# Kernel optimization log

Hardware: AMD Instinct MI355X
Metric: run time of the kernel (lower is better)

The kernel has to match this reference:

```python
import jax, jax.numpy as jnp
import numpy as np

GROUPS = 32
EPS = 1e-5


def setup_inputs() -> dict:
    key = jax.random.key(0)
    ks = jax.random.split(key, 4)
    n, c, h, w = 4, 512, 64, 64
    x = jax.random.normal(ks[0], (n, c, h, w), dtype=jnp.float32)
    gn_scale = jnp.ones((c,), dtype=jnp.float32)
    gn_bias = jnp.zeros((c,), dtype=jnp.float32)
    w_in = jax.random.normal(ks[1], (3 * c, c), dtype=jnp.float32) * (1.0 / np.sqrt(c))
    b_in = jnp.zeros((3 * c,), dtype=jnp.float32)
    w_out = jax.random.normal(ks[2], (c, c), dtype=jnp.float32) * (1.0 / np.sqrt(c))
    b_out = jnp.zeros((c,), dtype=jnp.float32)
    return {"x": x, "gn_scale": gn_scale, "gn_bias": gn_bias,
            "w_in": w_in, "b_in": b_in, "w_out": w_out, "b_out": b_out}


def reference(x, gn_scale, gn_bias, w_in, b_in, w_out, b_out):
    n, c, h, w = x.shape
    # GroupNorm(32, c): normalize over (c//32, h, w) per group
    xg = x.reshape(n, GROUPS, -1)
    mean = xg.mean(axis=-1, keepdims=True)
    var = xg.var(axis=-1, keepdims=True)
    xn = ((xg - mean) * jax.lax.rsqrt(var + EPS)).reshape(n, c, h, w)
    xn = xn * gn_scale[:, None, None] + gn_bias[:, None, None]
    # [n, c, h, w] -> [n, hw, c]
    seq = xn.reshape(n, c, h * w).transpose(0, 2, 1)
    # fused qkv projection
    qkv = jnp.einsum('nsc,dc->nsd', seq, w_in) + b_in  # [n, hw, 3c]
    q, k, v = jnp.split(qkv, 3, axis=-1)
    # single head, head_dim = c
    scale = 1.0 / jnp.sqrt(jnp.asarray(c, dtype=x.dtype))
    scores = jnp.einsum('nsc,ntc->nst', q, k) * scale  # [n, hw, hw]
    attn = jax.nn.softmax(scores, axis=-1)
    out = jnp.einsum('nst,ntc->nsc', attn, v)
    out = jnp.einsum('nsc,dc->nsd', out, w_out) + b_out
    out = out.transpose(0, 2, 1).reshape(n, c, h, w)
    return out + x
```

## Files before the change

### kernel.cpp

```cpp
#include <hip/hip_runtime.h>
#include <hip/hip_bf16.h>

#define NBATCH 4
#define C 512
#define HW 4096
#define GROUPS 32
#define EPSV 1e-5f
#define ATTN_SCALE_L2 0.0637587085f

typedef short bf16x8 __attribute__((ext_vector_type(8)));
typedef float f32x4 __attribute__((ext_vector_type(4)));

__device__ __forceinline__ float bf(unsigned short u) {
  return __uint_as_float(((unsigned)u) << 16);
}
__device__ __forceinline__ unsigned short fb(float v) {
  __hip_bfloat16 h = __float2bfloat16(v);
  return *(unsigned short*)&h;
}
__device__ __forceinline__ bf16x8 frag_ld(const short* p) {
  return *(const bf16x8*)p;
}
#define MFMA(a, b, c) __builtin_amdgcn_mfma_f32_16x16x32_bf16((a), (b), (c), 0, 0, 0)

#define SCHED_FENCE() __builtin_amdgcn_sched_barrier(0)
#define BAR()                                   \
  do {                                          \
    asm volatile("" ::: "memory");              \
    SCHED_FENCE();                              \
    __builtin_amdgcn_s_barrier();               \
    SCHED_FENCE();                              \
    asm volatile("" ::: "memory");              \
  } while (0)
#define WAITV(N)                                                  \
  do {                                                            \
    asm volatile("s_waitcnt vmcnt(" #N ")" ::: "memory");         \
    SCHED_FENCE();                                                \
  } while (0)
#define WAITLGKM()                                                \
  do {                                                            \
    asm volatile("s_waitcnt lgkmcnt(0)" ::: "memory");            \
    SCHED_FENCE();                                                \
  } while (0)

__device__ __forceinline__ void gl_lds16(const short* g, short* l) {
  __builtin_amdgcn_global_load_lds(
      (const __attribute__((address_space(1))) unsigned int*)g,
      (__attribute__((address_space(3))) unsigned int*)l, 16, 0, 0);
}

__device__ __forceinline__ void unpack8(uint4 w, float* f) {
  f[0] = __uint_as_float(w.x << 16);
  f[1] = __uint_as_float(w.x & 0xFFFF0000u);
  f[2] = __uint_as_float(w.y << 16);
  f[3] = __uint_as_float(w.y & 0xFFFF0000u);
  f[4] = __uint_as_float(w.z << 16);
  f[5] = __uint_as_float(w.z & 0xFFFF0000u);
  f[6] = __uint_as_float(w.w << 16);
  f[7] = __uint_as_float(w.w & 0xFFFF0000u);
}

__device__ __forceinline__ bool detect_f32(const void* w_in) {
  const unsigned short* u = (const unsigned short*)w_in;
  bool f32 = false;
#pragma unroll
  for (int i = 0; i < 64; ++i) {
    float v = bf(u[i]);
    if (!(fabsf(v) < 1e3f)) f32 = true;
  }
  return f32;
}
__device__ __forceinline__ float ld(const void* p, size_t i, bool f32) {
  if (f32) return ((const float*)p)[i];
  return bf(((const unsigned short*)p)[i]);
}

__device__ __forceinline__ void stage_xn(short* xn, const void* x,
                                         const void* gsc, const void* gbi,
                                         const float* stats, int nn, int t0,
                                         bool f32) {
  const int tid = threadIdx.x;
  const int part = tid & 3, crel = tid >> 2;
  for (int c0 = 0; c0 < 512; c0 += 64) {
    int c = c0 + crel;
    float rr = stats[128 + nn * GROUPS + (c >> 4)];
    float mu = stats[nn * GROUPS + (c >> 4)];
    float scl = ld(gsc, c, f32) * rr;
    float sft = ld(gbi, c, f32) - mu * scl;
    float f[8];
    if (f32) {
      const float4* p = (const float4*)((const float*)x +
                                        ((size_t)(nn * C + c) << 12) + t0 + part * 8);
      float4 r0 = p[0], r1 = p[1];
      f[0] = r0.x; f[1] = r0.y; f[2] = r0.z; f[3] = r0.w;
      f[4] = r1.x; f[5] = r1.y; f[6] = r1.z; f[7] = r1.w;
    } else {
      uint4 raw = *(const uint4*)((const unsigned short*)x +
                                  ((size_t)(nn * C + c) << 12) + t0 + part * 8);
      unpack8(raw, f);
    }
#pragma unroll
    for (int j = 0; j < 8; ++j)
      xn[(part * 8 + j) * 520 + c] = (short)fb(f[j] * scl + sft);
  }
}

__global__ __launch_bounds__(256) void gn_stats_kernel(
    const void* __restrict__ x, const void* __restrict__ w_in,
    float* __restrict__ stats) {
  const bool f32 = detect_f32(w_in);
  const int b = blockIdx.x;
  const size_t base = (size_t)b << 16;
  float s = 0.f, ss = 0.f;
  for (int i = threadIdx.x; i < 65536; i += 256) {
    float v = ld(x, base + i, f32);
    s += v;
    ss += v * v;
  }
  __shared__ float rs[256], rq[256];
  rs[threadIdx.x] = s;
  rq[threadIdx.x] = ss;
  __syncthreads();
  for (int off = 128; off > 0; off >>= 1) {
    if (threadIdx.x < off) {
      rs[threadIdx.x] += rs[threadIdx.x + off];
      rq[threadIdx.x] += rq[threadIdx.x + off];
    }
    __syncthreads();
  }
  if (threadIdx.x == 0) {
    float m = rs[0] * (1.0f / 65536.0f);
    float var = rq[0] * (1.0f / 65536.0f) - m * m;
    stats[b] = m;
    stats[128 + b] = rsqrtf(var + EPSV);
  }
}

__global__ __launch_bounds__(256) void wconv_kernel(
    const void* __restrict__ w_in, const void* __restrict__ w_out,
    short* __restrict__ wbf) {
  const bool f32 = detect_f32(w_in);
  size_t i = ((size_t)blockIdx.x * 256 + threadIdx.x) * 4;
  const void* src;
  size_t off;
  if (i < 786432) {
    src = w_in;
    off = i;
  } else {
    src = w_out;
    off = i - 786432;
  }
  if (f32) {
    float4 v = *(const float4*)((const float*)src + off);
    uint2 u;
    u.x = (unsigned)fb(v.x) | ((unsigned)fb(v.y) << 16);
    u.y = (unsigned)fb(v.z) | ((unsigned)fb(v.w) << 16);
    *(uint2*)(wbf + i) = u;
  } else {
    *(uint2*)(wbf + i) = *(const uint2*)((const unsigned short*)src + off);
  }
}

__global__ __launch_bounds__(256) void kv_gemm_kernel(
    const void* __restrict__ x, const void* __restrict__ gsc,
    const void* __restrict__ gbi, const float* __restrict__ stats,
    const void* __restrict__ w_in, const void* __restrict__ b_in,
    const short* __restrict__ wbf, unsigned short* __restrict__ kvbase,
    int nn0) {
  const bool f32 = detect_f32(w_in);
  const int nn = nn0 + blockIdx.z;
  unsigned short* kbuf = kvbase + (size_t)blockIdx.z * 4194304;
  unsigned short* vbuf = kbuf + 2097152;
  __shared__ __align__(16) short xn[32 * 520];
  const int tid = threadIdx.x;
  const int wave = tid >> 6, lane = tid & 63, l15 = lane & 15, quad = lane >> 4;
  const int t0 = blockIdx.y * 32;
  const int proj = blockIdx.x >> 1;
  const int ehalf = blockIdx.x & 1;

  stage_xn(xn, x, gsc, gbi, stats, nn, t0, f32);
  __syncthreads();

  const int wrow = 512 + proj * 512 + ehalf * 256 + wave * 64;
  const int cbase = ehalf * 256 + wave * 64;

  f32x4 acc[4][2];
#pragma unroll
  for (int i = 0; i < 4; ++i) {
    acc[i][0] = {0.f, 0.f, 0.f, 0.f};
    acc[i][1] = {0.f, 0.f, 0.f, 0.f};
  }

  for (int kc = 0; kc < 16; ++kc) {
    bf16x8 b0f = frag_ld(xn + l15 * 520 + kc * 32 + quad * 8);
    bf16x8 b1f = frag_ld(xn + (16 + l15) * 520 + kc * 32 + quad * 8);
#pragma unroll
    for (int es = 0; es < 4; ++es) {
      bf16x8 a = frag_ld(wbf + (size_t)(wrow + es * 16 + l15) * 512 + kc * 32 + quad * 8);
      acc[es][0] = MFMA(a, b0f, acc[es][0]);
      acc[es][1] = MFMA(a, b1f, acc[es][1]);
    }
  }

#pragma unroll
  for (int es = 0; es < 4; ++es) {
    int bidx = wrow + es * 16 + quad * 4;
    float b0 = ld(b_in, bidx, f32), b1 = ld(b_in, bidx + 1, f32);
    float b2 = ld(b_in, bidx + 2, f32), b3 = ld(b_in, bidx + 3, f32);
    int ecol = cbase + es * 16 + quad * 4;
#pragma unroll
    for (int ts = 0; ts < 2; ++ts) {
      int t = t0 + ts * 16 + l15;
      float vr[4] = {acc[es][ts][0] + b0, acc[es][ts][1] + b1,
                     acc[es][ts][2] + b2, acc[es][ts][3] + b3};
      if (proj == 0) {
        int sw = (((ecol >> 3) ^ (t & 7)) << 3) | (ecol & 7);
        uint2 u;
        u.x = (unsigned)fb(vr[0]) | ((unsigned)fb(vr[1]) << 16);
        u.y = (unsigned)fb(vr[2]) | ((unsigned)fb(vr[3]) << 16);
        *(uint2*)(kbuf + (size_t)t * 512 + sw) = u;
      } else {
        size_t tb = (size_t)(t >> 5) * 16384;
        int trel = t & 31;
#pragma unroll
        for (int i = 0; i < 4; ++i) {
          int e = ecol + i;
          vbuf[tb + (size_t)e * 32 + ((((trel >> 3) ^ ((e >> 1) & 3)) << 3)) +
               (trel & 7)] = fb(vr[i]);
        }
      }
    }
  }
}

__global__ __launch_bounds__(256, 2) void flash32_kernel(
    const void* __restrict__ x, const void* __restrict__ gsc,
    const void* __restrict__ gbi, const float* __restrict__ stats,
    const void* __restrict__ w_in, const void* __restrict__ b_in,
    const short* __restrict__ wbf, const short* __restrict__ wbfo,
    const unsigned short* __restrict__ kvbase,
    const void* __restrict__ b_out, void* __restrict__ out, int nn0,
    int conc) {
  const bool f32 = detect_f32(w_in);
  int nn, t0, slot;
  if (conc) {
    int xcd = blockIdx.x & 7;
    nn = xcd >> 1;
    slot = nn;
    t0 = ((((xcd & 1) << 6) | (blockIdx.x >> 3))) << 5;
  } else {
    nn = nn0; slot = 0; t0 = blockIdx.x << 5;
  }
  const unsigned short* kbuf = kvbase + (size_t)slot * 4194304;
  const unsigned short* vbuf = kbuf + 2097152;

  __shared__ __align__(16) short lds[35200];
  short* RA = lds;
  short* RB = lds + 16640;
  short* Ps = lds + 33280;
  float* hmf = (float*)(lds + 34560);
  float* lbf = (float*)(lds + 35072);
  const int tid = threadIdx.x;
  const int wave = tid >> 6, lane = tid & 63, l15 = lane & 15, quad = lane >> 4;
  const int th = wave & 1;
  const int qh = wave >> 1;

  bf16x8 q[16];
  stage_xn(RA, x, gsc, gbi, stats, nn, t0, f32);
  __syncthreads();
  {
    f32x4 qacc[8][2];
#pragma unroll
    for (int i = 0; i < 8; ++i) {
      qacc[i][0] = {0.f, 0.f, 0.f, 0.f};
      qacc[i][1] = {0.f, 0.f, 0.f, 0.f};
    }
    for (int kc = 0; kc < 16; ++kc) {
      bf16x8 bx0 = frag_ld(RA + l15 * 520 + kc * 32 + quad * 8);
      bf16x8 bx1 = frag_ld(RA + (16 + l15) * 520 + kc * 32 + quad * 8);
#pragma unroll
      for (int es = 0; es < 8; ++es) {
        bf16x8 a = frag_ld(wbf + (size_t)(wave * 128 + es * 16 + l15) * 512 + kc * 32 + quad * 8);
        qacc[es][0] = MFMA(a, bx0, qacc[es][0]);
        qacc[es][1] = MFMA(a, bx1, qacc[es][1]);
      }
    }
#pragma unroll
    for (int es = 0; es < 8; ++es) {
      int e0 = wave * 128 + es * 16 + quad * 4;
      float b0 = ld(b_in, e0, f32), b1 = ld(b_in, e0 + 1, f32);
      float b2 = ld(b_in, e0 + 2, f32), b3 = ld(b_in, e0 + 3, f32);
#pragma unroll
      for (int ts = 0; ts < 2; ++ts) {
        int t = ts * 16 + l15;
        uint2 u;
        u.x = (unsigned)fb((qacc[es][ts][0] + b0) * ATTN_SCALE_L2) |
              ((unsigned)fb((qacc[es][ts][1] + b1) * ATTN_SCALE_L2) << 16);
        u.y = (unsigned)fb((qacc[es][ts][2] + b2) * ATTN_SCALE_L2) |
              ((unsigned)fb((qacc[es][ts][3] + b3) * ATTN_SCALE_L2) << 16);
        *(uint2*)(RB + t * 520 + e0) = u;
      }
    }
    __syncthreads();
#pragma unroll
    for (int kc = 0; kc < 16; ++kc)
      q[kc] = frag_ld(RB + (qh * 16 + l15) * 520 + kc * 32 + quad * 8);
    __syncthreads();
  }

#define STAGE_K(tk)                                                           \
  {                                                                           \
    const short* s_ = (const short*)kbuf + (size_t)(tk)*16384 + wave * 4096 + \
                      lane * 8;                                               \
    short* d_ = RA + wave * 4096;                                             \
    _Pragma("unroll") for (int i_ = 0; i_ < 8; ++i_)                          \
        gl_lds16(s_ + i_ * 512, d_ + i_ * 512);                               \
  }
#define STAGE_V(tk)                                                           \
  {                                                                           \
    const short* s_ = (const short*)vbuf + (size_t)(tk)*16384 + wave * 4096 + \
                      lane * 8;                                               \
    short* d_ = RB + wave * 4096;                                             \
    _Pragma("unroll") for (int i_ = 0; i_ < 8; ++i_)                          \
        gl_lds16(s_ + i_ * 512, d_ + i_ * 512);                               \
  }

  f32x4 o[2][8];
#pragma unroll
  for (int hh = 0; hh < 2; ++hh)
#pragma unroll
    for (int et = 0; et < 8; ++et) o[hh][et] = {0.f, 0.f, 0.f, 0.f};
  float mrow2[2] = {-3.0e38f, -3.0e38f};
  float lpart = 0.f;

  STAGE_K(0);
  STAGE_V(0);

  for (int tk = 0; tk < 128; ++tk) {
    WAITV(8);
    BAR();

    f32x4 sA = {0.f, 0.f, 0.f, 0.f}, sB = {0.f, 0.f, 0.f, 0.f};
    __builtin_amdgcn_s_setprio(1);
#pragma unroll
    for (int kc = 0; kc < 16; kc += 2) {
      int g0 = ((kc * 4 + quad) ^ (l15 & 7)) * 8;
      int g1 = (((kc + 1) * 4 + quad) ^ (l15 & 7)) * 8;
      bf16x8 kb0 = frag_ld(RA + (th * 16 + l15) * 512 + g0);
      bf16x8 kb1 = frag_ld(RA + (th * 16 + l15) * 512 + g1);
      sA = MFMA(kb0, q[kc], sA);
      sB = MFMA(kb1, q[kc + 1], sB);
    }
    __builtin_amdgcn_s_setprio(0);
    f32x4 s = sA + sB;
    float hm = fmaxf(fmaxf(s[0], s[1]), fmaxf(s[2], s[3]));
    hmf[th * 128 + (qh * 16 + l15) * 4 + quad] = hm;
    WAITLGKM();
    BAR();
    if (tk < 127) STAGE_K(tk + 1);

    float4 a0 = *(const float4*)&hmf[l15 * 4];
    float4 a1 = *(const float4*)&hmf[128 + l15 * 4];
    float4 c0 = *(const float4*)&hmf[(16 + l15) * 4];
    float4 c1 = *(const float4*)&hmf[128 + (16 + l15) * 4];
    float m0 = fmaxf(fmaxf(fmaxf(a0.x, a0.y), fmaxf(a0.z, a0.w)),
                     fmaxf(fmaxf(a1.x, a1.y), fmaxf(a1.z, a1.w)));
    float m1 = fmaxf(fmaxf(fmaxf(c0.x, c0.y), fmaxf(c0.z, c0.w)),
                     fmaxf(fmaxf(c1.x, c1.y), fmaxf(c1.z, c1.w)));
    bool grow = (m0 > mrow2[0]) | (m1 > mrow2[1]);
    if (__any(grow)) {
      float n0 = fmaxf(mrow2[0], m0), n1 = fmaxf(mrow2[1], m1);
      float sc0 = exp2f(mrow2[0] - n0), sc1 = exp2f(mrow2[1] - n1);
      mrow2[0] = n0;
      mrow2[1] = n1;
      lpart *= (qh ? sc1 : sc0);
#pragma unroll
      for (int et = 0; et < 8; ++et) {
        o[0][et] *= sc0;
        o[1][et] *= sc1;
      }
    }
    float mq = qh ? mrow2[1] : mrow2[0];
    float p0 = exp2f(s[0] - mq), p1 = exp2f(s[1] - mq);
    float p2 = exp2f(s[2] - mq), p3 = exp2f(s[3] - mq);
    lpart += (p0 + p1) + (p2 + p3);
    uint2 u;
    u.x = (unsigned)fb(p0) | ((unsigned)fb(p1) << 16);
    u.y = (unsigned)fb(p2) | ((unsigned)fb(p3) << 16);
    *(uint2*)(Ps + (qh * 16 + l15) * 40 + th * 16 + quad * 4) = u;
    WAITLGKM();
    if (tk == 127) { WAITV(0); } else { WAITV(8); }
    BAR();

    bf16x8 pa0 = frag_ld(Ps + l15 * 40 + quad * 8);
    bf16x8 pa1 = frag_ld(Ps + (16 + l15) * 40 + quad * 8);
    __builtin_amdgcn_s_setprio(1);
#pragma unroll
    for (int et = 0; et < 8; ++et) {
      int e = wave * 128 + et * 16 + l15;
      bf16x8 vb = frag_ld(RB + e * 32 + ((quad ^ ((l15 >> 1) & 3)) << 3));
      o[0][et] = MFMA(vb, pa0, o[0][et]);
      o[1][et] = MFMA(vb, pa1, o[1][et]);
    }
    __builtin_amdgcn_s_setprio(0);
    BAR();
    if (tk < 127) STAGE_V(tk + 1);
  }

  lpart += __shfl_xor(lpart, 16);
  lpart += __shfl_xor(lpart, 32);
  if (quad == 0) lbf[th * 32 + qh * 16 + l15] = lpart;
  __syncthreads();
  float inv0 = 1.0f / (lbf[l15] + lbf[32 + l15]);
  float inv1 = 1.0f / (lbf[16 + l15] + lbf[48 + l15]);

#pragma unroll
  for (int et = 0; et < 8; ++et) {
    uint2 u0, u1;
    u0.x = (unsigned)fb(o[0][et][0] * inv0) | ((unsigned)fb(o[0][et][1] * inv0) << 16);
    u0.y = (unsigned)fb(o[0][et][2] * inv0) | ((unsigned)fb(o[0][et][3] * inv0) << 16);
    u1.x = (unsigned)fb(o[1][et][0] * inv1) | ((unsigned)fb(o[1][et][1] * inv1) << 16);
    u1.y = (unsigned)fb(o[1][et][2] * inv1) | ((unsigned)fb(o[1][et][3] * inv1) << 16);
    int ecol = wave * 128 + et * 16 + quad * 4;
    *(uint2*)(lds + (l15)*520 + ecol) = u0;
    *(uint2*)(lds + (16 + l15) * 520 + ecol) = u1;
  }
  __syncthreads();

  f32x4 oa[8][2];
#pragma unroll
  for (int i = 0; i < 8; ++i) {
    oa[i][0] = {0.f, 0.f, 0.f, 0.f};
    oa[i][1] = {0.f, 0.f, 0.f, 0.f};
  }
  for (int kc = 0; kc < 16; ++kc) {
    bf16x8 ob0 = frag_ld(lds + l15 * 520 + kc * 32 + quad * 8);
    bf16x8 ob1 = frag_ld(lds + (16 + l15) * 520 + kc * 32 + quad * 8);
#pragma unroll
    for (int es = 0; es < 8; ++es) {
      bf16x8 a = frag_ld(wbfo + (size_t)(wave * 128 + es * 16 + l15) * 512 + kc * 32 + quad * 8);
      oa[es][0] = MFMA(a, ob0, oa[es][0]);
      oa[es][1] = MFMA(a, ob1, oa[es][1]);
    }
  }
#pragma unroll
  for (int es = 0; es < 8; ++es) {
    int cc = wave * 128 + es * 16 + quad * 4;
    float b0 = ld(b_out, cc, f32), b1 = ld(b_out, cc + 1, f32);
    float b2 = ld(b_out, cc + 2, f32), b3 = ld(b_out, cc + 3, f32);
#pragma unroll
    for (int ts = 0; ts < 2; ++ts) {
      int t = t0 + ts * 16 + l15;
      float vr[4] = {oa[es][ts][0] + b0, oa[es][ts][1] + b1,
                     oa[es][ts][2] + b2, oa[es][ts][3] + b3};
#pragma unroll
      for (int r = 0; r < 4; ++r) {
        size_t oidx = ((size_t)(nn * C + cc + r) << 12) + t;
        float v = vr[r] + ld(x, oidx, f32);
        if (f32)
          ((float*)out)[oidx] = v;
        else
          ((unsigned short*)out)[oidx] = fb(v);
      }
    }
  }
}

extern "C" void kernel_launch(void* const* d_in, const int* in_sizes, int n_in,
                              void* d_out, int out_size, void* d_ws, size_t ws_size,
                              hipStream_t stream) {
  const void* x = d_in[0];
  const void* gn_scale = d_in[1];
  const void* gn_bias = d_in[2];
  const void* w_in = d_in[3];
  const void* b_in = d_in[4];
  const void* w_out = d_in[5];
  const void* b_out = d_in[6];
  (void)in_sizes; (void)n_in; (void)out_size;

  float* stats = (float*)d_ws;
  unsigned short* kv0 = (unsigned short*)((char*)d_ws + 1024);
  const size_t slotB = 8388608;
  const size_t need4 = 1024 + 4 * slotB + 2097152;

  gn_stats_kernel<<<NBATCH * GROUPS, 256, 0, stream>>>(x, w_in, stats);

  if (ws_size >= need4) {
    short* wbf = (short*)((char*)d_ws + 1024 + 4 * slotB);
    wconv_kernel<<<1024, 256, 0, stream>>>(w_in, w_out, wbf);
    kv_gemm_kernel<<<dim3(4, 128, 4), 256, 0, stream>>>(
        x, gn_scale, gn_bias, stats, w_in, b_in, wbf, kv0, 0);
    flash32_kernel<<<dim3(512), 256, 0, stream>>>(
        x, gn_scale, gn_bias, stats, w_in, b_in, wbf, wbf + 786432, kv0,
        b_out, d_out, 0, 1);
  } else {
    short* wbf = (short*)((char*)d_ws + 1024 + slotB);
    wconv_kernel<<<1024, 256, 0, stream>>>(w_in, w_out, wbf);
    for (int nn = 0; nn < NBATCH; ++nn) {
      kv_gemm_kernel<<<dim3(4, 128, 1), 256, 0, stream>>>(
          x, gn_scale, gn_bias, stats, w_in, b_in, wbf, kv0, nn);
      flash32_kernel<<<dim3(128), 256, 0, stream>>>(
          x, gn_scale, gn_bias, stats, w_in, b_in, wbf, wbf + 786432, kv0,
          b_out, d_out, nn, 0);
    }
  }
}
```

Baseline: 590.8 us.

## Compute full K and V per block and stage outputs through LDS for coalesced stores

Each kv_gemm block now computes all 1024 K/V output columns for its 32 tokens instead of a quarter. The normalized-input staging (GroupNorm plus transpose into LDS) therefore runs once per token tile rather than four times, and the grid shrinks by four. Results are written into the shared buffer in the swizzled layout and then copied out with 16-byte coalesced stores, replacing the scattered 2-byte V stores. The cost is 128 accumulator registers per thread (with launch bounds asking for 2 blocks per SM), fewer blocks in flight, and extra barriers.

```diff
diff --git a/kernel.cpp b/kernel.cpp
--- a/kernel.cpp
+++ b/kernel.cpp
@@ -161,32 +161,29 @@
   }
 }
 
-__global__ __launch_bounds__(256) void kv_gemm_kernel(
+__global__ __launch_bounds__(256, 2) void kv_gemm_kernel(
     const void* __restrict__ x, const void* __restrict__ gsc,
     const void* __restrict__ gbi, const float* __restrict__ stats,
     const void* __restrict__ w_in, const void* __restrict__ b_in,
     const short* __restrict__ wbf, unsigned short* __restrict__ kvbase,
     int nn0) {
   const bool f32 = detect_f32(w_in);
-  const int nn = nn0 + blockIdx.z;
-  unsigned short* kbuf = kvbase + (size_t)blockIdx.z * 4194304;
+  const int nn = nn0 + blockIdx.y;
+  unsigned short* kbuf = kvbase + (size_t)blockIdx.y * 4194304;
   unsigned short* vbuf = kbuf + 2097152;
   __shared__ __align__(16) short xn[32 * 520];
   const int tid = threadIdx.x;
   const int wave = tid >> 6, lane = tid & 63, l15 = lane & 15, quad = lane >> 4;
-  const int t0 = blockIdx.y * 32;
-  const int proj = blockIdx.x >> 1;
-  const int ehalf = blockIdx.x & 1;
+  const int t0 = blockIdx.x * 32;
 
   stage_xn(xn, x, gsc, gbi, stats, nn, t0, f32);
   __syncthreads();
 
-  const int wrow = 512 + proj * 512 + ehalf * 256 + wave * 64;
-  const int cbase = ehalf * 256 + wave * 64;
-
-  f32x4 acc[4][2];
-#pragma unroll
-  for (int i = 0; i < 4; ++i) {
+  const int wbase = 512 + wave * 256;
+
+  f32x4 acc[16][2];
+#pragma unroll
+  for (int i = 0; i < 16; ++i) {
     acc[i][0] = {0.f, 0.f, 0.f, 0.f};
     acc[i][1] = {0.f, 0.f, 0.f, 0.f};
   }
@@ -195,40 +192,71 @@
     bf16x8 b0f = frag_ld(xn + l15 * 520 + kc * 32 + quad * 8);
     bf16x8 b1f = frag_ld(xn + (16 + l15) * 520 + kc * 32 + quad * 8);
 #pragma unroll
-    for (int es = 0; es < 4; ++es) {
-      bf16x8 a = frag_ld(wbf + (size_t)(wrow + es * 16 + l15) * 512 + kc * 32 + quad * 8);
+    for (int es = 0; es < 16; ++es) {
+      bf16x8 a = frag_ld(wbf + (size_t)(wbase + es * 16 + l15) * 512 + kc * 32 + quad * 8);
       acc[es][0] = MFMA(a, b0f, acc[es][0]);
       acc[es][1] = MFMA(a, b1f, acc[es][1]);
     }
   }
-
-#pragma unroll
-  for (int es = 0; es < 4; ++es) {
-    int bidx = wrow + es * 16 + quad * 4;
-    float b0 = ld(b_in, bidx, f32), b1 = ld(b_in, bidx + 1, f32);
-    float b2 = ld(b_in, bidx + 2, f32), b3 = ld(b_in, bidx + 3, f32);
-    int ecol = cbase + es * 16 + quad * 4;
-#pragma unroll
-    for (int ts = 0; ts < 2; ++ts) {
-      int t = t0 + ts * 16 + l15;
-      float vr[4] = {acc[es][ts][0] + b0, acc[es][ts][1] + b1,
-                     acc[es][ts][2] + b2, acc[es][ts][3] + b3};
-      if (proj == 0) {
-        int sw = (((ecol >> 3) ^ (t & 7)) << 3) | (ecol & 7);
+  __syncthreads();
+
+  if (wave < 2) {
+#pragma unroll
+    for (int es = 0; es < 16; ++es) {
+      int bidx = wbase + es * 16 + quad * 4;
+      float b0 = ld(b_in, bidx, f32), b1 = ld(b_in, bidx + 1, f32);
+      float b2 = ld(b_in, bidx + 2, f32), b3 = ld(b_in, bidx + 3, f32);
+      int ecol = wave * 256 + es * 16 + quad * 4;
+#pragma unroll
+      for (int ts = 0; ts < 2; ++ts) {
+        int trel = ts * 16 + l15;
+        int sw = (((ecol >> 3) ^ (trel & 7)) << 3) | (ecol & 7);
         uint2 u;
-        u.x = (unsigned)fb(vr[0]) | ((unsigned)fb(vr[1]) << 16);
-        u.y = (unsigned)fb(vr[2]) | ((unsigned)fb(vr[3]) << 16);
-        *(uint2*)(kbuf + (size_t)t * 512 + sw) = u;
-      } else {
-        size_t tb = (size_t)(t >> 5) * 16384;
-        int trel = t & 31;
+        u.x = (unsigned)fb(acc[es][ts][0] + b0) |
+              ((unsigned)fb(acc[es][ts][1] + b1) << 16);
+        u.y = (unsigned)fb(acc[es][ts][2] + b2) |
+              ((unsigned)fb(acc[es][ts][3] + b3) << 16);
+        *(uint2*)(xn + trel * 512 + sw) = u;
+      }
+    }
+  }
+  __syncthreads();
+  {
+    short* dst = (short*)kbuf + (size_t)t0 * 512;
+#pragma unroll
+    for (int j = 0; j < 8; ++j) {
+      int idx = (j * 256 + tid) * 8;
+      *(uint4*)(dst + idx) = *(const uint4*)(xn + idx);
+    }
+  }
+  __syncthreads();
+
+  if (wave >= 2) {
+#pragma unroll
+    for (int es = 0; es < 16; ++es) {
+      int bidx = wbase + es * 16 + quad * 4;
+      float bb[4] = {ld(b_in, bidx, f32), ld(b_in, bidx + 1, f32),
+                     ld(b_in, bidx + 2, f32), ld(b_in, bidx + 3, f32)};
+      int ecol = (wave - 2) * 256 + es * 16 + quad * 4;
+#pragma unroll
+      for (int ts = 0; ts < 2; ++ts) {
+        int trel = ts * 16 + l15;
 #pragma unroll
         for (int i = 0; i < 4; ++i) {
           int e = ecol + i;
-          vbuf[tb + (size_t)e * 32 + ((((trel >> 3) ^ ((e >> 1) & 3)) << 3)) +
-               (trel & 7)] = fb(vr[i]);
+          xn[e * 32 + ((((trel >> 3) ^ ((e >> 1) & 3)) << 3)) + (trel & 7)] =
+              fb(acc[es][ts][i] + bb[i]);
         }
       }
+    }
+  }
+  __syncthreads();
+  {
+    short* dst = (short*)vbuf + (size_t)(t0 >> 5) * 16384;
+#pragma unroll
+    for (int j = 0; j < 8; ++j) {
+      int idx = (j * 256 + tid) * 8;
+      *(uint4*)(dst + idx) = *(const uint4*)(xn + idx);
     }
   }
 }
@@ -488,7 +516,7 @@
   if (ws_size >= need4) {
     short* wbf = (short*)((char*)d_ws + 1024 + 4 * slotB);
     wconv_kernel<<<1024, 256, 0, stream>>>(w_in, w_out, wbf);
-    kv_gemm_kernel<<<dim3(4, 128, 4), 256, 0, stream>>>(
+    kv_gemm_kernel<<<dim3(128, 4), 256, 0, stream>>>(
         x, gn_scale, gn_bias, stats, w_in, b_in, wbf, kv0, 0);
     flash32_kernel<<<dim3(512), 256, 0, stream>>>(
         x, gn_scale, gn_bias, stats, w_in, b_in, wbf, wbf + 786432, kv0,
@@ -497,7 +525,7 @@
     short* wbf = (short*)((char*)d_ws + 1024 + slotB);
     wconv_kernel<<<1024, 256, 0, stream>>>(w_in, w_out, wbf);
     for (int nn = 0; nn < NBATCH; ++nn) {
-      kv_gemm_kernel<<<dim3(4, 128, 1), 256, 0, stream>>>(
+      kv_gemm_kernel<<<dim3(128, 1), 256, 0, stream>>>(
           x, gn_scale, gn_bias, stats, w_in, b_in, wbf, kv0, nn);
       flash32_kernel<<<dim3(128), 256, 0, stream>>>(
           x, gn_scale, gn_bias, stats, w_in, b_in, wbf, wbf + 786432, kv0,
```

Result: no change. 585.0 us (-1.0%).
